# Kernel tuning notes

Measured on AMD Instinct MI355X. Metric: run time of the kernel, lower is better.

## Reference

```python
import jax, jax.numpy as jnp
import numpy as np

V, D, H, NQ = 32000, 768, 12, 768
B, S = 2, 1024
HD = D // H

def conv1d(x, w, b, pad):
    # x [B,C,L], w [O,I,K]
    y = jax.lax.conv_general_dilated(x, w, (1,), [(pad, pad)], dimension_numbers=('NCH', 'OIH', 'NCH'))
    return y + b[None, :, None]

def maxpool3(x):
    return jax.lax.reduce_window(x, -jnp.inf, jax.lax.max, (1, 1, 3), (1, 1, 1), [(0, 0), (0, 0), (1, 1)])

def ln(x, g, b):
    m = jnp.mean(x, -1, keepdims=True)
    v = jnp.mean((x - m) ** 2, -1, keepdims=True)
    return (x - m) * jax.lax.rsqrt(v + 1e-5) * g + b

def setup_inputs():
    key = jax.random.key(0)
    ks = iter(jax.random.split(key, 64))
    def w(shape, s=0.02):
        return jax.random.normal(next(ks), shape, jnp.float32) * s
    inp = {}
    inp['x'] = jax.random.randint(next(ks), (B, S), 0, V)
    inp['attention_mask'] = jax.random.randint(next(ks), (B, S), 0, 2, dtype=jnp.int32)
    inp['adj_matrix'] = jax.random.uniform(next(ks), (B, S, S), jnp.float32) * (1.0 / S)
    inp['emb'] = w((V, D))
    inp['inc1_w'] = w((64, D, 1)); inp['inc1_b'] = jnp.zeros((64,))
    inp['inc3a_w'] = w((96, D, 1)); inp['inc3a_b'] = jnp.zeros((96,))
    inp['inc3b_w'] = w((128, 96, 3)); inp['inc3b_b'] = jnp.zeros((128,))
    inp['inc5a_w'] = w((16, D, 1)); inp['inc5a_b'] = jnp.zeros((16,))
    inp['inc5b_w'] = w((32, 16, 5)); inp['inc5b_b'] = jnp.zeros((32,))
    inp['incp_w'] = w((32, D, 1)); inp['incp_b'] = jnp.zeros((32,))
    inp['q_rot'] = jax.random.normal(next(ks), (2, NQ, 3), jnp.float32)
    inp['q_ent'] = jax.random.normal(next(ks), (2, NQ - 1), jnp.float32)
    inp['gnn_w1'] = w((D, D // 2)); inp['gnn_b1'] = jnp.zeros((D // 2,))
    inp['gnn_w2'] = w((D // 2, D)); inp['gnn_b2'] = jnp.zeros((D,))
    inp['wq'] = w((D, D)); inp['bq'] = jnp.zeros((D,))
    inp['wk'] = w((D, D)); inp['bk'] = jnp.zeros((D,))
    inp['wv'] = w((D, D)); inp['bv'] = jnp.zeros((D,))
    inp['wo'] = w((D, D)); inp['bo'] = jnp.zeros((D,))
    inp['ff_w1'] = w((D, 4 * D)); inp['ff_b1'] = jnp.zeros((4 * D,))
    inp['ff_w2'] = w((4 * D, D)); inp['ff_b2'] = jnp.zeros((D,))
    inp['ln1_g'] = jnp.ones((D,)); inp['ln1_b'] = jnp.zeros((D,))
    inp['ln2_g'] = jnp.ones((D,)); inp['ln2_b'] = jnp.zeros((D,))
    inp['out_w'] = w((D, V)); inp['out_b'] = jnp.zeros((V,))
    inp['task_w'] = w((D, 3)); inp['task_b'] = jnp.zeros((3,))
    return inp

def reference(x, attention_mask, adj_matrix, emb, inc1_w, inc1_b, inc3a_w, inc3a_b, inc3b_w, inc3b_b, inc5a_w, inc5a_b, inc5b_w, inc5b_b, incp_w, incp_b, q_rot, q_ent, gnn_w1, gnn_b1, gnn_w2, gnn_b2, wq, bq, wk, bk, wv, bv, wo, bo, ff_w1, ff_b1, ff_w2, ff_b2, ln1_g, ln1_b, ln2_g, ln2_b, out_w, out_b, task_w, task_b):
    h = emb[x]                      # [B,S,D]
    hc = h.transpose(0, 2, 1)       # [B,D,S]
    b1 = conv1d(hc, inc1_w, inc1_b, 0)
    b3 = conv1d(conv1d(hc, inc3a_w, inc3a_b, 0), inc3b_w, inc3b_b, 1)
    b5 = conv1d(conv1d(hc, inc5a_w, inc5a_b, 0), inc5b_w, inc5b_b, 2)
    bp = conv1d(maxpool3(hc), incp_w, incp_b, 0)
    h = jnp.concatenate([b1, b3, b5, bp], axis=1).transpose(0, 2, 1)  # [B,S,256]
    # quantum layer: pad 256 -> NQ
    h = jnp.pad(h, ((0, 0), (0, 0), (0, NQ - h.shape[-1])))
    for layer in range(2):
        h = jnp.sin(h[..., None] + q_rot[layer]).sum(-1)          # [B,S,NQ]
        hs = jnp.roll(h, 1, axis=-1)
        h = h[..., :-1] * jnp.sin(q_ent[layer]) + hs[..., :-1] * jnp.cos(q_ent[layer])
        h = jnp.pad(h, ((0, 0), (0, 0), (0, 1)))
    # GNN
    g = jax.nn.relu(jnp.matmul(adj_matrix, h) @ gnn_w1 + gnn_b1)
    h = jnp.matmul(adj_matrix, g) @ gnn_w2 + gnn_b2
    # attention (faithful to original mask-bug: masks where transformed mask == 0)
    am = (1.0 - attention_mask.astype(jnp.float32))[:, None, None, :] * -10000.0
    Q = (h @ wq + bq).reshape(B, S, H, HD).transpose(0, 2, 1, 3)
    K = (h @ wk + bk).reshape(B, S, H, HD).transpose(0, 2, 1, 3)
    Vv = (h @ wv + bv).reshape(B, S, H, HD).transpose(0, 2, 1, 3)
    scores = jnp.einsum('bhqd,bhkd->bhqk', Q, K) / jnp.sqrt(jnp.float32(HD))
    scores = jnp.where(am == 0.0, -1e9, scores)
    attn = jax.nn.softmax(scores, axis=-1)
    ctx = jnp.einsum('bhqk,bhkd->bhqd', attn, Vv).transpose(0, 2, 1, 3).reshape(B, S, D)
    h = ln(h + (ctx @ wo + bo), ln1_g, ln1_b)
    ff = jax.nn.relu(h @ ff_w1 + ff_b1) @ ff_w2 + ff_b2
    h = ln(h + ff, ln2_g, ln2_b)
    token_output = h @ out_w + out_b            # [B,S,V]
    task_output = h.mean(axis=1) @ task_w + task_b  # [B,3]
    return token_output, task_output
```

## Files before the change

### kernel.cpp

```cpp
#include <hip/hip_runtime.h>
#include <hip/hip_bf16.h>

#define B_ 2
#define S_ 1024
#define D_ 768
#define H_ 12
#define HD_ 64
#define V_ 32000
#define NQ_ 768
#define NTOK (B_*S_)
#define QKVS 1572864L

typedef __attribute__((ext_vector_type(8))) short short8;
typedef __attribute__((ext_vector_type(4))) short s16x4;
typedef __attribute__((ext_vector_type(4))) float f32x4;
typedef __attribute__((ext_vector_type(4))) int i32x4;

typedef const __attribute__((address_space(1))) void* as1vp;
typedef __attribute__((address_space(3))) void* as3vp;

__device__ __forceinline__ short f2bf(float f) {
    union { float f; unsigned u; } v; v.f = f;
    unsigned r = (v.u + 0x7FFFu + ((v.u >> 16) & 1u)) >> 16;
    return (short)r;
}
__device__ __forceinline__ float b2fs(short s) {
    union { unsigned u; float f; } v; v.u = ((unsigned)(unsigned short)s) << 16;
    return v.f;
}

__global__ void k_embed2(const int* __restrict__ x, const float* __restrict__ emb,
                         short* __restrict__ h0b, short* __restrict__ mpb) {
    int n = blockIdx.x; int s = n & (S_-1);
    int r0 = x[n];
    int rm = (s > 0)      ? x[n-1] : -1;
    int rp = (s < S_-1)   ? x[n+1] : -1;
    for (int d = threadIdx.x; d < D_; d += blockDim.x) {
        float e = emb[(long)r0*D_ + d];
        float m = e;
        if (rm >= 0) m = fmaxf(m, emb[(long)rm*D_ + d]);
        if (rp >= 0) m = fmaxf(m, emb[(long)rp*D_ + d]);
        h0b[(long)n*D_ + d] = f2bf(e);
        mpb[(long)n*D_ + d] = f2bf(m);
    }
}

__global__ __launch_bounds__(256) void k_mix(
    const float* __restrict__ CO, const float* __restrict__ c3w,
    const float* __restrict__ c3b, const float* __restrict__ c5w,
    const float* __restrict__ c5b, const float* __restrict__ q_rot,
    const float* __restrict__ q_ent, float* __restrict__ h1f)
{
    __shared__ float co[5][176];
    __shared__ float ta[NQ_];
    __shared__ float tb[NQ_];
    int n = blockIdx.x; int s = n & (S_-1);
    int t = threadIdx.x;
    for (int idx = t; idx < 5*176; idx += 256) {
        int dr = idx / 176 - 2, c = idx % 176;
        int ss = s + dr;
        co[idx/176][c] = (ss >= 0 && ss < S_) ? CO[(long)(n + dr)*176 + c] : 0.f;
    }
    for (int d = 256 + t; d < NQ_; d += 256) ta[d] = 0.f;
    __syncthreads();
    if (t < 64) {
        ta[t] = co[2][t];
    } else if (t < 192) {
        int o = t - 64;
        float acc = c3b[o];
        #pragma unroll
        for (int k = 0; k < 3; k++)
            for (int i = 0; i < 96; i++)
                acc += co[1+k][64+i] * c3w[(o*96+i)*3 + k];
        ta[t] = acc;
    } else if (t < 224) {
        int o = t - 192;
        float acc = c5b[o];
        #pragma unroll
        for (int k = 0; k < 5; k++)
            for (int i = 0; i < 16; i++)
                acc += co[k][160+i] * c5w[(o*16+i)*5 + k];
        ta[t] = acc;
    } else {
        ta[t] = h1f[(long)n*NQ_ + t];
    }
    __syncthreads();
    #pragma unroll
    for (int layer = 0; layer < 2; layer++) {
        const float* rot = q_rot + (long)layer*NQ_*3;
        const float* ent = q_ent + (long)layer*(NQ_-1);
        for (int q = t; q < NQ_; q += 256) {
            float hv = ta[q];
            tb[q] = __sinf(hv + rot[q*3]) + __sinf(hv + rot[q*3+1]) + __sinf(hv + rot[q*3+2]);
        }
        __syncthreads();
        for (int q = t; q < NQ_; q += 256) {
            float v;
            if (q == NQ_-1) v = 0.f;
            else {
                int qm = (q == 0) ? (NQ_-1) : (q-1);
                v = tb[q]*__sinf(ent[q]) + tb[qm]*__cosf(ent[q]);
            }
            ta[q] = v;
        }
        __syncthreads();
    }
    for (int q = t; q < NQ_; q += 256) h1f[(long)n*NQ_ + q] = ta[q];
}

template<int AMODE, int OMODE, bool RELU, int KSPLIT = 1>
__global__ __launch_bounds__(256) void k_bgemm(
    const short* __restrict__ A, const short* __restrict__ Bm,
    void* __restrict__ Cv, float* __restrict__ C2,
    const float* __restrict__ bias, float scale,
    int N, int K, int lda, int ldb, int ldc,
    long sA, long sB, long sC)
{
    __shared__ short lds[2][8192];
    const int t = threadIdx.x;
    const int lane = t & 63, wave = t >> 6;
    const int wm = wave >> 1, wn = wave & 1;
    const int l15 = lane & 15, l4 = lane >> 4;

    int bx = blockIdx.x, by = blockIdx.y;
    if (KSPLIT == 1 && gridDim.z == 1) {
        int lin = by * gridDim.x + bx;
        int nwg = gridDim.x * gridDim.y;
        int xcd = lin & 7, pos = lin >> 3;
        int q = nwg >> 3, r = nwg & 7;
        int lin2 = (xcd < r ? xcd*(q+1) : r*(q+1) + (xcd-r)*q) + pos;
        bx = lin2 % gridDim.x;
        by = lin2 / gridDim.x;
    }
    const int tile_m = bx * 128, tile_n = by * 128;
    const int kz = (KSPLIT > 1) ? blockIdx.z : 0;
    const int Keff = K / KSPLIT;
    const int kbase = kz * Keff;
    const long aoff = (KSPLIT > 1) ? 0 : (long)blockIdx.z * sA;
    const long boff = (KSPLIT > 1) ? 0 : (long)blockIdx.z * sB;
    const long coff = (KSPLIT > 1) ? 0 : (long)blockIdx.z * sC;

    const int cA0 = t, cA1 = t + 256;
    const int arow0 = tile_m + ((cA0 >> 6) << 4) + (cA0 & 15);
    const int arow1 = tile_m + ((cA1 >> 6) << 4) + (cA1 & 15);
    const int akb0 = ((cA0 >> 4) & 3) * 8;
    const int akb1 = ((cA1 >> 4) & 3) * 8;
    const int bcol0 = tile_n + (((cA0 >> 4) & 7) << 4) + (cA0 & 15);
    const int bcol1 = tile_n + (((cA1 >> 4) & 7) << 4) + (cA1 & 15);
    const int bkb0 = (cA0 >> 7) * 8;
    const int bkb1 = (cA1 >> 7) * 8;
    const short* bp0 = Bm + boff + (long)bcol0*ldb + bkb0 + kbase;
    const short* bp1 = Bm + boff + (long)bcol1*ldb + bkb1 + kbase;
    const short* ap0 = nullptr; const short* ap1 = nullptr;
    long abase0 = 0, abase1 = 0;
    if (AMODE == 0) {
        ap0 = A + aoff + (long)arow0*lda + akb0 + kbase;
        ap1 = A + aoff + (long)arow1*lda + akb1 + kbase;
    } else {
        abase0 = ((long)((arow0 >> 10)*H_) * S_ + (arow0 & (S_-1))) * 64;
        abase1 = ((long)((arow1 >> 10)*H_) * S_ + (arow1 & (S_-1))) * 64;
    }
    const int wb = wave * 1024;

    auto stage = [&](int buf, int k0) {
        char* lb = (char*)&lds[buf][0];
        const short *a0, *a1;
        if (AMODE == 0) { a0 = ap0 + k0; a1 = ap1 + k0; }
        else {
            int ka0 = kbase + k0 + akb0, ka1 = kbase + k0 + akb1;
            a0 = A + abase0 + (long)(ka0 >> 6)*(S_*64) + (ka0 & 63);
            a1 = A + abase1 + (long)(ka1 >> 6)*(S_*64) + (ka1 & 63);
        }
        __builtin_amdgcn_global_load_lds((as1vp)a0,          (as3vp)(lb + wb),          16, 0, 0);
        __builtin_amdgcn_global_load_lds((as1vp)a1,          (as3vp)(lb + 4096 + wb),   16, 0, 0);
        __builtin_amdgcn_global_load_lds((as1vp)(bp0 + k0),  (as3vp)(lb + 8192 + wb),   16, 0, 0);
        __builtin_amdgcn_global_load_lds((as1vp)(bp1 + k0),  (as3vp)(lb + 12288 + wb),  16, 0, 0);
    };

    f32x4 acc[4][4] = {};
    const int nk = Keff >> 5;
    stage(0, 0);
    __syncthreads();
    int cur = 0;
    for (int ks = 0; ks < nk; ks++) {
        if (ks + 1 < nk) stage(cur ^ 1, (ks + 1) << 5);
        short8 af[4], bfv[4];
        const short* lb = &lds[cur][0];
        #pragma unroll
        for (int m = 0; m < 4; m++)
            af[m] = *(const short8*)(lb + (wm*4 + m)*512 + l4*128 + l15*8);
        #pragma unroll
        for (int n = 0; n < 4; n++)
            bfv[n] = *(const short8*)(lb + 4096 + l4*1024 + (wn*4 + n)*128 + l15*8);
        #pragma unroll
        for (int m = 0; m < 4; m++)
            #pragma unroll
            for (int n = 0; n < 4; n++)
                acc[m][n] = __builtin_amdgcn_mfma_f32_16x16x32_bf16(af[m], bfv[n], acc[m][n], 0, 0, 0);
        __syncthreads();
        cur ^= 1;
    }

    #pragma unroll
    for (int m = 0; m < 4; m++) {
        #pragma unroll
        for (int n = 0; n < 4; n++) {
            int col = tile_n + wn*64 + n*16 + l15;
            if (col >= N) continue;
            float bv = (bias && (KSPLIT == 1 || kz == 0)) ? bias[col] : 0.f;
            #pragma unroll
            for (int r = 0; r < 4; r++) {
                int row = tile_m + wm*64 + m*16 + l4*4 + r;
                float v = acc[m][n][r] * scale + bv;
                if (RELU) v = fmaxf(v, 0.f);
                if (OMODE == 0) {
                    if (KSPLIT > 1)
                        atomicAdd(&((float*)Cv)[(long)row*ldc + col], v);
                    else
                        ((float*)Cv)[coff + (long)row*ldc + col] = v;
                } else if (OMODE == 1) {
                    ((short*)Cv)[coff + (long)row*ldc + col] = f2bf(v);
                } else if (OMODE == 2) {
                    C2[coff + (long)row*ldc + col] = v;
                    ((short*)Cv)[coff + (long)row*ldc + col] = f2bf(v);
                } else {
                    int seg = (col >= 1536) ? 2 : ((col >= 768) ? 1 : 0);
                    int c = col - seg*768;
                    int hh = c >> 6, dd = c & 63;
                    int b = row >> 10, s = row & (S_-1);
                    long hidx = (long)(b*H_ + hh);
                    short* base = (short*)Cv;
                    if (seg < 2) base[(long)seg*QKVS + (hidx*S_ + s)*64 + dd] = f2bf(v);
                    else         base[2L*QKVS + (hidx*64 + dd)*S_ + s] = f2bf(v);
                }
            }
        }
    }
}

__global__ __launch_bounds__(512, 1) void k_vgemm(
    const short* __restrict__ A, const short* __restrict__ Bm,
    float* __restrict__ C, const float* __restrict__ bias,
    int N, int K, int lda, int ldb, int ldc)
{
    extern __shared__ short lds[];
    const int t = threadIdx.x;
    const int lane = t & 63, wave = t >> 6;
    const int wm = wave >> 2, wn = wave & 3;
    const int l15 = lane & 15, l4 = lane >> 4;
    int bx = blockIdx.x, by = blockIdx.y;
    {
        int lin = by * gridDim.x + bx;
        int nwg = gridDim.x * gridDim.y;
        int xcd = lin & 7, pos = lin >> 3;
        int q = nwg >> 3, r = nwg & 7;
        int lin2 = (xcd < r ? xcd*(q+1) : r*(q+1) + (xcd-r)*q) + pos;
        bx = lin2 % gridDim.x; by = lin2 / gridDim.x;
    }
    const int tile_m = bx * 256, tile_n = by * 256;

    const int c0 = wave*128 + lane;
    const int c1 = c0 + 64;
    const int ar0 = ((c0 >> 6) << 4) + (c0 & 15), ak0 = ((c0 >> 4) & 3) << 3;
    const int ar1 = ((c1 >> 6) << 4) + (c1 & 15), ak1 = ((c1 >> 4) & 3) << 3;
    const short* pa0 = A + (long)(tile_m + ar0)*lda + ak0;
    const short* pa1 = A + (long)(tile_m + ar1)*lda + ak1;
    const short* pb0 = Bm + (long)(tile_n + ar0)*ldb + ak0;
    const short* pb1 = Bm + (long)(tile_n + ar1)*ldb + ak1;
    char* lb = (char*)lds;
    const int wb0 = wave*2048, wb1 = wave*2048 + 1024;

    auto stage = [&](int reg, int s) {
        int k = s << 5;
        char* ab = lb + reg*32768;
        __builtin_amdgcn_global_load_lds((as1vp)(pa0 + k), (as3vp)(ab + wb0),         16, 0, 0);
        __builtin_amdgcn_global_load_lds((as1vp)(pa1 + k), (as3vp)(ab + wb1),         16, 0, 0);
        __builtin_amdgcn_global_load_lds((as1vp)(pb0 + k), (as3vp)(ab + 16384 + wb0), 16, 0, 0);
        __builtin_amdgcn_global_load_lds((as1vp)(pb1 + k), (as3vp)(ab + 16384 + wb1), 16, 0, 0);
    };

    f32x4 acc[8][4] = {};
    const int nks = K >> 5;
    stage(0, 0); stage(1, 1); stage(2, 2);
    const int ard = ((wm*8) << 10) + (l4 << 8) + l15*16;
    const int brd = 16384 + ((wn*4) << 10) + (l4 << 8) + l15*16;

    int reg = 0;
    for (int s = 0; s < nks; s++) {
        if (s + 3 < nks) {
            int r3 = reg + 3; if (r3 >= 5) r3 -= 5;
            stage(r3, s + 3);
        }
        if (s < nks - 3)       asm volatile("s_waitcnt vmcnt(12)" ::: "memory");
        else if (s == nks - 3) asm volatile("s_waitcnt vmcnt(8)"  ::: "memory");
        else if (s == nks - 2) asm volatile("s_waitcnt vmcnt(4)"  ::: "memory");
        else                   asm volatile("s_waitcnt vmcnt(0)"  ::: "memory");
        __builtin_amdgcn_s_barrier();
        const char* rb = lb + reg*32768;
        short8 a[8], b[4];
        #pragma unroll
        for (int fr = 0; fr < 8; fr++) a[fr] = *(const short8*)(rb + ard + (fr << 10));
        #pragma unroll
        for (int fc = 0; fc < 4; fc++) b[fc] = *(const short8*)(rb + brd + (fc << 10));
        __builtin_amdgcn_s_setprio(1);
        #pragma unroll
        for (int fr = 0; fr < 8; fr++)
            #pragma unroll
            for (int fc = 0; fc < 4; fc++)
                acc[fr][fc] = __builtin_amdgcn_mfma_f32_16x16x32_bf16(a[fr], b[fc], acc[fr][fc], 0, 0, 0);
        __builtin_amdgcn_s_setprio(0);
        if (++reg == 5) reg = 0;
    }

    #pragma unroll
    for (int fr = 0; fr < 8; fr++) {
        #pragma unroll
        for (int fc = 0; fc < 4; fc++) {
            int col = tile_n + wn*64 + fc*16 + l15;
            float bv = bias ? bias[col] : 0.f;
            #pragma unroll
            for (int rr = 0; rr < 4; rr++) {
                int row = tile_m + wm*128 + fr*16 + l4*4 + rr;
                C[(long)row*ldc + col] = acc[fr][fc][rr] + bv;
            }
        }
    }
}

__global__ __launch_bounds__(256) void k_fattn(
    const short* __restrict__ Q, const short* __restrict__ K,
    const short* __restrict__ Vt, const int* __restrict__ mask,
    short* __restrict__ ctx)
{
    __shared__ short plds[4096];
    const int t = threadIdx.x;
    const int lane = t & 63, wave = t >> 6;
    const int l15 = lane & 15, l4 = lane >> 4;
    const int qt = blockIdx.x, z = blockIdx.y;
    const int b = z / H_;
    const long zb = (long)z * S_ * 64;

    const int q = qt*64 + wave*16 + l15;
    short8 aq0 = *(const short8*)(Q + zb + (long)q*64 + l4*8);
    short8 aq1 = *(const short8*)(Q + zb + (long)q*64 + l4*8 + 32);

    float m[4] = {-1e30f, -1e30f, -1e30f, -1e30f};
    float l[4] = {0.f, 0.f, 0.f, 0.f};
    f32x4 O[4] = {};
    short* pw = plds + wave*1024;

    for (int kt = 0; kt < 16; kt++) {
        const int kvb = kt*64;
        f32x4 s[4] = {};
        #pragma unroll
        for (int ct = 0; ct < 4; ct++) {
            const short* kp = K + zb + (long)(kvb + ct*16 + l15)*64 + l4*8;
            short8 b0 = *(const short8*)(kp);
            short8 b1 = *(const short8*)(kp + 32);
            s[ct] = __builtin_amdgcn_mfma_f32_16x16x32_bf16(aq0, b0, s[ct], 0, 0, 0);
            s[ct] = __builtin_amdgcn_mfma_f32_16x16x32_bf16(aq1, b1, s[ct], 0, 0, 0);
        }
        float p[4][4];
        float rmax[4] = {-1e30f, -1e30f, -1e30f, -1e30f};
        #pragma unroll
        for (int ct = 0; ct < 4; ct++) {
            int mv = mask[b*S_ + kvb + ct*16 + l15];
            #pragma unroll
            for (int r = 0; r < 4; r++) {
                float v = (mv == 1) ? -1e9f : s[ct][r]*0.125f;
                p[ct][r] = v;
                rmax[r] = fmaxf(rmax[r], v);
            }
        }
        #pragma unroll
        for (int r = 0; r < 4; r++) {
            float v = rmax[r];
            v = fmaxf(v, __shfl_xor(v, 1));
            v = fmaxf(v, __shfl_xor(v, 2));
            v = fmaxf(v, __shfl_xor(v, 4));
            v = fmaxf(v, __shfl_xor(v, 8));
            float mn = fmaxf(m[r], v);
            float corr = __expf(m[r] - mn);
            float srow = 0.f;
            #pragma unroll
            for (int ct = 0; ct < 4; ct++) {
                float e = __expf(p[ct][r] - mn);
                p[ct][r] = e;
                srow += e;
            }
            srow += __shfl_xor(srow, 1);
            srow += __shfl_xor(srow, 2);
            srow += __shfl_xor(srow, 4);
            srow += __shfl_xor(srow, 8);
            l[r] = l[r]*corr + srow;
            m[r] = mn;
            #pragma unroll
            for (int c2 = 0; c2 < 4; c2++) O[c2][r] *= corr;
        }
        #pragma unroll
        for (int ct = 0; ct < 4; ct++)
            #pragma unroll
            for (int r = 0; r < 4; r++)
                pw[(l4*4 + r)*64 + ct*16 + l15] = f2bf(p[ct][r]);
        asm volatile("s_waitcnt lgkmcnt(0)" ::: "memory");
        __builtin_amdgcn_sched_barrier(0);
        short8 pa0 = *(const short8*)(pw + l15*64 + l4*8);
        short8 pa1 = *(const short8*)(pw + l15*64 + l4*8 + 32);
        #pragma unroll
        for (int c2 = 0; c2 < 4; c2++) {
            const short* vp = Vt + zb + (long)(c2*16 + l15)*S_ + kvb + l4*8;
            short8 v0 = *(const short8*)(vp);
            short8 v1 = *(const short8*)(vp + 32);
            O[c2] = __builtin_amdgcn_mfma_f32_16x16x32_bf16(pa0, v0, O[c2], 0, 0, 0);
            O[c2] = __builtin_amdgcn_mfma_f32_16x16x32_bf16(pa1, v1, O[c2], 0, 0, 0);
        }
    }
    #pragma unroll
    for (int r = 0; r < 4; r++) {
        float inv = 1.f / l[r];
        int qo = qt*64 + wave*16 + l4*4 + r;
        #pragma unroll
        for (int c2 = 0; c2 < 4; c2++)
            ctx[zb + (long)qo*64 + c2*16 + l15] = f2bf(O[c2][r] * inv);
    }
}

struct WPArgs {
    const float *ow, *wq, *wk, *wv, *wo, *g1, *g2, *f1, *f2, *adj;
    const float *w1, *w3, *w5, *wp, *b1, *b3, *b5, *bq, *bk, *bv;
    short *owt, *wqkvt, *gw1t, *gw2t, *fw1t, *fw2t, *adjb, *wincat, *wincp;
    float *binc, *bqkv;
};
__global__ __launch_bounds__(256) void k_wprep(WPArgs a) {
    __shared__ float tile[32][33];
    int blk = blockIdx.x, t = threadIdx.x;
    const float* src; short* dst;
    int R, C, bx, by;
    if (blk < 24000)      { src = a.ow; dst = a.owt; R = 768; C = 32000; bx = blk % 1000; by = blk / 1000; }
    else if (blk < 26304) { int r = blk - 24000; int z = r / 576; r %= 576;
        src = (z == 0) ? a.wq : (z == 1) ? a.wk : (z == 2) ? a.wv : a.wo;
        dst = a.wqkvt + (long)z*589824; R = 768; C = 768; bx = r % 24; by = r / 24; }
    else if (blk < 26592) { int r = blk - 26304; src = a.g1; dst = a.gw1t; R = 768; C = 384;  bx = r % 12; by = r / 12; }
    else if (blk < 26880) { int r = blk - 26592; src = a.g2; dst = a.gw2t; R = 384; C = 768;  bx = r % 24; by = r / 24; }
    else if (blk < 29184) { int r = blk - 26880; src = a.f1; dst = a.fw1t; R = 768; C = 3072; bx = r % 96; by = r / 96; }
    else if (blk < 31488) { int r = blk - 29184; src = a.f2; dst = a.fw2t; R = 3072; C = 768; bx = r % 24; by = r / 24; }
    else if (blk < 33536) {
        long i = ((long)(blk - 31488)*256 + t)*4;
        f32x4 v = *(const f32x4*)(a.adj + i);
        a.adjb[i+0] = f2bf(v.x); a.adjb[i+1] = f2bf(v.y);
        a.adjb[i+2] = f2bf(v.z); a.adjb[i+3] = f2bf(v.w);
        return;
    } else {
        int r = blk - 33536;
        const float* s2; short* d2; long base;
        if (r < 48)       { s2 = a.w1; d2 = a.wincat;          base = (long)r*1024; }
        else if (r < 120) { s2 = a.w3; d2 = a.wincat + 49152;  base = (long)(r-48)*1024; }
        else if (r < 132) { s2 = a.w5; d2 = a.wincat + 122880; base = (long)(r-120)*1024; }
        else if (r < 156) { s2 = a.wp; d2 = a.wincp;           base = (long)(r-132)*1024; }
        else {
            if (t < 176) a.binc[t] = (t < 64) ? a.b1[t] : (t < 160 ? a.b3[t-64] : a.b5[t-160]);
            for (int i = t; i < 2304; i += 256)
                a.bqkv[i] = (i < 768) ? a.bq[i] : (i < 1536 ? a.bk[i-768] : a.bv[i-1536]);
            return;
        }
        long i = base + (long)t*4;
        f32x4 v = *(const f32x4*)(s2 + i);
        d2[i+0] = f2bf(v.x); d2[i+1] = f2bf(v.y); d2[i+2] = f2bf(v.z); d2[i+3] = f2bf(v.w);
        return;
    }
    int bc = bx*32, br = by*32;
    int tx = t & 31, ty = t >> 5;
    #pragma unroll
    for (int i = 0; i < 32; i += 8)
        tile[ty + i][tx] = src[(long)(br + ty + i)*C + bc + tx];
    __syncthreads();
    #pragma unroll
    for (int i = 0; i < 32; i += 8)
        dst[(long)(bc + ty + i)*R + br + tx] = f2bf(tile[tx][ty + i]);
}

template<bool RELU>
__global__ void k_t2b(const float* __restrict__ in, short* __restrict__ out,
                      int R, int C, long sIn, long sOut) {
    __shared__ float tile[32][33];
    int bc = blockIdx.x * 32, br = blockIdx.y * 32;
    const float* ip = in + (long)blockIdx.z * sIn;
    short* op = out + (long)blockIdx.z * sOut;
    int tx = threadIdx.x & 31, ty = threadIdx.x >> 5;
    #pragma unroll
    for (int i = 0; i < 32; i += 8)
        tile[ty + i][tx] = ip[(long)(br + ty + i)*C + bc + tx];
    __syncthreads();
    #pragma unroll
    for (int i = 0; i < 32; i += 8) {
        float v = tile[tx][ty + i];
        if (RELU) v = fmaxf(v, 0.f);
        op[(long)(bc + ty + i)*R + br + tx] = f2bf(v);
    }
}

__global__ void k_addln(const float* __restrict__ a, const float* __restrict__ bvec,
                        const float* __restrict__ g, const float* __restrict__ be,
                        float* __restrict__ outf, short* __restrict__ outb) {
    __shared__ float row[D_];
    __shared__ float red[256];
    int n = blockIdx.x, t = threadIdx.x;
    float lsum = 0.f;
    for (int d = t; d < D_; d += 256) {
        float v = a[(long)n*D_ + d] + bvec[(long)n*D_ + d];
        row[d] = v; lsum += v;
    }
    red[t] = lsum; __syncthreads();
    for (int off = 128; off > 0; off >>= 1) {
        if (t < off) red[t] += red[t+off];
        __syncthreads();
    }
    float mean = red[0] / D_; __syncthreads();
    float lvar = 0.f;
    for (int d = t; d < D_; d += 256) { float v = row[d]-mean; lvar += v*v; }
    red[t] = lvar; __syncthreads();
    for (int off = 128; off > 0; off >>= 1) {
        if (t < off) red[t] += red[t+off];
        __syncthreads();
    }
    float rstd = rsqrtf(red[0]/D_ + 1e-5f);
    for (int d = t; d < D_; d += 256) {
        float v = (row[d]-mean)*rstd*g[d] + be[d];
        if (outf) outf[(long)n*D_ + d] = v;
        outb[(long)n*D_ + d] = f2bf(v);
    }
}

__global__ __launch_bounds__(256) void k_pool(const short* __restrict__ h,
                                              float* __restrict__ pooled) {
    int blk = blockIdx.x;
    int b = blk >> 4, ch = blk & 15;
    int t = threadIdx.x;
    float s0 = 0.f, s1 = 0.f, s2 = 0.f;
    for (int ss = ch*64; ss < ch*64 + 64; ss++) {
        const short* row = h + (long)(b*S_ + ss)*D_;
        s0 += b2fs(row[t]);
        s1 += b2fs(row[t + 256]);
        s2 += b2fs(row[t + 512]);
    }
    atomicAdd(&pooled[b*D_ + t],       s0 * (1.f/S_));
    atomicAdd(&pooled[b*D_ + t + 256], s1 * (1.f/S_));
    atomicAdd(&pooled[b*D_ + t + 512], s2 * (1.f/S_));
}

__global__ __launch_bounds__(256) void k_task(const float* __restrict__ pooled,
                                              const float* __restrict__ tw,
                                              const float* __restrict__ tb,
                                              float* __restrict__ out) {
    __shared__ float red[256][3];
    int b = blockIdx.x, t = threadIdx.x;
    float a0 = 0.f, a1 = 0.f, a2 = 0.f;
    for (int d = t; d < D_; d += 256) {
        float p = pooled[b*D_ + d];
        a0 += p*tw[d*3+0]; a1 += p*tw[d*3+1]; a2 += p*tw[d*3+2];
    }
    red[t][0] = a0; red[t][1] = a1; red[t][2] = a2;
    __syncthreads();
    for (int off = 128; off > 0; off >>= 1) {
        if (t < off) {
            red[t][0] += red[t+off][0];
            red[t][1] += red[t+off][1];
            red[t][2] += red[t+off][2];
        }
        __syncthreads();
    }
    if (t < 3) out[(long)NTOK*V_ + b*3 + t] = red[0][t] + tb[t];
}

extern "C" void kernel_launch(void* const* d_in, const int* in_sizes, int n_in,
                              void* d_out, int out_size, void* d_ws, size_t ws_size,
                              hipStream_t stream) {
    const int*   x      = (const int*)d_in[0];
    const int*   amask  = (const int*)d_in[1];
    const float* adj    = (const float*)d_in[2];
    const float* emb    = (const float*)d_in[3];
    const float* inc1_w = (const float*)d_in[4];  const float* inc1_b = (const float*)d_in[5];
    const float* inc3a_w= (const float*)d_in[6];  const float* inc3a_b= (const float*)d_in[7];
    const float* inc3b_w= (const float*)d_in[8];  const float* inc3b_b= (const float*)d_in[9];
    const float* inc5a_w= (const float*)d_in[10]; const float* inc5a_b= (const float*)d_in[11];
    const float* inc5b_w= (const float*)d_in[12]; const float* inc5b_b= (const float*)d_in[13];
    const float* incp_w = (const float*)d_in[14]; const float* incp_b = (const float*)d_in[15];
    const float* q_rot  = (const float*)d_in[16]; const float* q_ent  = (const float*)d_in[17];
    const float* gnn_w1 = (const float*)d_in[18]; const float* gnn_b1 = (const float*)d_in[19];
    const float* gnn_w2 = (const float*)d_in[20]; const float* gnn_b2 = (const float*)d_in[21];
    const float* wq = (const float*)d_in[22]; const float* bq = (const float*)d_in[23];
    const float* wk = (const float*)d_in[24]; const float* bk = (const float*)d_in[25];
    const float* wv = (const float*)d_in[26]; const float* bv = (const float*)d_in[27];
    const float* wo = (const float*)d_in[28]; const float* bo = (const float*)d_in[29];
    const float* ff_w1 = (const float*)d_in[30]; const float* ff_b1 = (const float*)d_in[31];
    const float* ff_w2 = (const float*)d_in[32]; const float* ff_b2 = (const float*)d_in[33];
    const float* ln1_g = (const float*)d_in[34]; const float* ln1_b = (const float*)d_in[35];
    const float* ln2_g = (const float*)d_in[36]; const float* ln2_b = (const float*)d_in[37];
    const float* out_w = (const float*)d_in[38]; const float* out_b = (const float*)d_in[39];
    const float* task_w= (const float*)d_in[40]; const float* task_b= (const float*)d_in[41];

    float* F = (float*)d_out;
    short* wqkvt = (short*)(F + 0L);
    short* gw1t  = (short*)(F + 1179648L);
    short* gw2t  = (short*)(F + 1327104L);
    short* fw1t  = (short*)(F + 1474560L);
    short* fw2t  = (short*)(F + 2654208L);
    short* wincat= (short*)(F + 3833856L);
    short* wincp = (short*)(F + 3950592L);
    float* binc  = F + 4012032L;
    float* bqkv  = F + 4012288L;
    short* adjb  = (short*)(F + 4014592L);
    short* h0b   = (short*)(F + 5063168L);
    short* mpb   = (short*)(F + 5849600L);
    float* CO    = F + 6636032L;
    float* h1f   = F + 6996480L;
    short* h1t   = (short*)(F + 8569344L);
    short* t1b   = (short*)(F + 9355776L);
    float* gbf   = F + 10142208L;
    short* gt    = (short*)(F + 10928640L);
    short* t2bv  = (short*)(F + 11321856L);
    float* h2f   = F + 11715072L;
    short* h2b   = (short*)(F + 13287936L);
    short* Qh    = (short*)(F + 14074368L);
    short* Kh    = (short*)(F + 14860800L);
    short* Vt    = (short*)(F + 15647232L);
    short* ctxh  = (short*)(F + 16499200L);
    float* ao    = F + 17285632L;
    float* hlnf  = F + 18858496L;
    short* hlnb  = (short*)(F + 20431360L);
    short* ff1b  = (short*)(F + 21217792L);
    float* ao2   = F + 24363520L;

    char* W = (char*)d_ws;
    short* hfb    = (short*)(W + 0);
    float* pooled = (float*)(W + 3145728);
    short* owt    = (short*)(W + 3151872);

    auto gb = [](int M, int N, int Z) { return dim3((unsigned)(M/128), (unsigned)((N+127)/128), (unsigned)Z); };

    hipFuncSetAttribute((const void*)k_vgemm, hipFuncAttributeMaxDynamicSharedMemorySize, 163840);

    hipMemsetAsync(gbf, 0, (size_t)NTOK*384*4, stream);
    hipMemsetAsync(ao,  0, (size_t)NTOK*D_*4, stream);
    hipMemsetAsync(ao2, 0, (size_t)NTOK*D_*4, stream);
    hipMemsetAsync(CO,  0, (size_t)NTOK*176*4, stream);
    hipMemsetAsync(h1f, 0, (size_t)NTOK*NQ_*4, stream);
    hipMemsetAsync(pooled, 0, (size_t)B_*D_*4, stream);

    {
        WPArgs wa;
        wa.ow = out_w; wa.wq = wq; wa.wk = wk; wa.wv = wv; wa.wo = wo;
        wa.g1 = gnn_w1; wa.g2 = gnn_w2; wa.f1 = ff_w1; wa.f2 = ff_w2; wa.adj = adj;
        wa.w1 = inc1_w; wa.w3 = inc3a_w; wa.w5 = inc5a_w; wa.wp = incp_w;
        wa.b1 = inc1_b; wa.b3 = inc3a_b; wa.b5 = inc5a_b;
        wa.bq = bq; wa.bk = bk; wa.bv = bv;
        wa.owt = owt; wa.wqkvt = wqkvt; wa.gw1t = gw1t; wa.gw2t = gw2t;
        wa.fw1t = fw1t; wa.fw2t = fw2t; wa.adjb = adjb;
        wa.wincat = wincat; wa.wincp = wincp; wa.binc = binc; wa.bqkv = bqkv;
        k_wprep<<<dim3(33693), 256, 0, stream>>>(wa);
    }

    k_embed2<<<dim3(NTOK), dim3(256), 0, stream>>>(x, emb, h0b, mpb);

    k_bgemm<0,0,false,4><<<gb(NTOK, 176, 4), 256, 0, stream>>>(
        h0b, wincat, CO, nullptr, binc, 1.f, 176, D_, D_, D_, 176, 0, 0, 0);
    k_bgemm<0,0,false,8><<<gb(NTOK, 32, 8), 256, 0, stream>>>(
        mpb, wincp, h1f + 224, nullptr, incp_b, 1.f, 32, D_, D_, D_, NQ_, 0, 0, 0);

    k_mix<<<dim3(NTOK), dim3(256), 0, stream>>>(
        CO, inc3b_w, inc3b_b, inc5b_w, inc5b_b, q_rot, q_ent, h1f);

    k_t2b<false><<<dim3(24,32,2), 256, 0, stream>>>(h1f, h1t, S_, NQ_, (long)S_*NQ_, (long)S_*NQ_);
    k_bgemm<0,1,false><<<gb(S_, NQ_, B_), 256, 0, stream>>>(
        adjb, h1t, t1b, nullptr, nullptr, 1.f, NQ_, S_, S_, S_, NQ_,
        (long)S_*S_, (long)NQ_*S_, (long)S_*NQ_);
    k_bgemm<0,0,false,4><<<gb(NTOK, 384, 4), 256, 0, stream>>>(
        t1b, gw1t, gbf, nullptr, gnn_b1, 1.f, 384, D_, D_, D_, 384, 0, 0, 0);
    k_t2b<true><<<dim3(12,32,2), 256, 0, stream>>>(gbf, gt, S_, 384, (long)S_*384, (long)S_*384);
    k_bgemm<0,1,false><<<gb(S_, 384, B_), 256, 0, stream>>>(
        adjb, gt, t2bv, nullptr, nullptr, 1.f, 384, S_, S_, S_, 384,
        (long)S_*S_, (long)384*S_, (long)S_*384);
    k_bgemm<0,2,false><<<gb(NTOK, D_, 1), 256, 0, stream>>>(
        t2bv, gw2t, h2b, h2f, gnn_b2, 1.f, D_, 384, 384, 384, D_, 0, 0, 0);

    k_bgemm<0,5,false><<<gb(NTOK, 3*D_, 1), 256, 0, stream>>>(
        h2b, wqkvt, Qh, nullptr, bqkv, 1.f, 3*D_, D_, D_, D_, 0, 0, 0, 0);
    k_fattn<<<dim3(S_/64, B_*H_), 256, 0, stream>>>(Qh, Kh, Vt, amask, ctxh);
    k_bgemm<1,0,false,2><<<gb(NTOK, D_, 2), 256, 0, stream>>>(
        ctxh, wqkvt + 3L*589824, ao, nullptr, bo, 1.f, D_, D_, D_, D_, D_, 0, 0, 0);
    k_addln<<<dim3(NTOK), dim3(256), 0, stream>>>(h2f, ao, ln1_g, ln1_b, hlnf, hlnb);

    k_bgemm<0,1,true><<<gb(NTOK, 4*D_, 1), 256, 0, stream>>>(
        hlnb, fw1t, ff1b, nullptr, ff_b1, 1.f, 4*D_, D_, D_, D_, 4*D_, 0, 0, 0);
    k_bgemm<0,0,false,4><<<gb(NTOK, D_, 4), 256, 0, stream>>>(
        ff1b, fw2t, ao2, nullptr, ff_b2, 1.f, D_, 4*D_, 4*D_, 4*D_, D_, 0, 0, 0);
    k_addln<<<dim3(NTOK), dim3(256), 0, stream>>>(hlnf, ao2, ln2_g, ln2_b, nullptr, hfb);

    k_pool<<<dim3(B_*16), dim3(256), 0, stream>>>(hfb, pooled);
    k_vgemm<<<dim3(NTOK/256, V_/256, 1), dim3(512), 163840, stream>>>(
        hfb, owt, (float*)d_out, out_b, V_, D_, D_, D_, V_);
    k_task<<<dim3(B_), dim3(256), 0, stream>>>(pooled, task_w, task_b, (float*)d_out);
}
```

Before: 640.2 us.

## Restructure vocab GEMM pipeline to double-buffered 64-wide K phases

Replaces the five-slot, three-deep staged pipeline (32-wide K steps with fine-grained vmcnt waits) in the output-vocabulary GEMM with a two-buffer scheme. Each buffer holds a 64-wide K chunk, and each phase does one full wait and barrier, then runs two MFMA sub-steps. This halves the barrier count per K and cuts dynamic LDS from 160KB to 128KB. The trade is a shallower prefetch: each phase now waits for all outstanding loads (vmcnt 0), so memory latency may be less hidden.

New measurement: 650.1 us. No clear change (+1.6%).

```diff
diff --git a/kernel.cpp b/kernel.cpp
--- a/kernel.cpp
+++ b/kernel.cpp
@@ -270,46 +270,47 @@
     char* lb = (char*)lds;
     const int wb0 = wave*2048, wb1 = wave*2048 + 1024;
 
-    auto stage = [&](int reg, int s) {
-        int k = s << 5;
-        char* ab = lb + reg*32768;
-        __builtin_amdgcn_global_load_lds((as1vp)(pa0 + k), (as3vp)(ab + wb0),         16, 0, 0);
-        __builtin_amdgcn_global_load_lds((as1vp)(pa1 + k), (as3vp)(ab + wb1),         16, 0, 0);
-        __builtin_amdgcn_global_load_lds((as1vp)(pb0 + k), (as3vp)(ab + 16384 + wb0), 16, 0, 0);
-        __builtin_amdgcn_global_load_lds((as1vp)(pb1 + k), (as3vp)(ab + 16384 + wb1), 16, 0, 0);
+    auto stage = [&](int reg, int p) {
+        int k = p << 6;
+        char* ab = lb + reg*65536;
+        __builtin_amdgcn_global_load_lds((as1vp)(pa0 + k),      (as3vp)(ab + wb0),          16, 0, 0);
+        __builtin_amdgcn_global_load_lds((as1vp)(pa1 + k),      (as3vp)(ab + wb1),          16, 0, 0);
+        __builtin_amdgcn_global_load_lds((as1vp)(pa0 + k + 32), (as3vp)(ab + 16384 + wb0),  16, 0, 0);
+        __builtin_amdgcn_global_load_lds((as1vp)(pa1 + k + 32), (as3vp)(ab + 16384 + wb1),  16, 0, 0);
+        __builtin_amdgcn_global_load_lds((as1vp)(pb0 + k),      (as3vp)(ab + 32768 + wb0),  16, 0, 0);
+        __builtin_amdgcn_global_load_lds((as1vp)(pb1 + k),      (as3vp)(ab + 32768 + wb1),  16, 0, 0);
+        __builtin_amdgcn_global_load_lds((as1vp)(pb0 + k + 32), (as3vp)(ab + 49152 + wb0),  16, 0, 0);
+        __builtin_amdgcn_global_load_lds((as1vp)(pb1 + k + 32), (as3vp)(ab + 49152 + wb1),  16, 0, 0);
     };
 
     f32x4 acc[8][4] = {};
-    const int nks = K >> 5;
-    stage(0, 0); stage(1, 1); stage(2, 2);
+    const int nph = K >> 6;
+    stage(0, 0);
     const int ard = ((wm*8) << 10) + (l4 << 8) + l15*16;
-    const int brd = 16384 + ((wn*4) << 10) + (l4 << 8) + l15*16;
-
-    int reg = 0;
-    for (int s = 0; s < nks; s++) {
-        if (s + 3 < nks) {
-            int r3 = reg + 3; if (r3 >= 5) r3 -= 5;
-            stage(r3, s + 3);
-        }
-        if (s < nks - 3)       asm volatile("s_waitcnt vmcnt(12)" ::: "memory");
-        else if (s == nks - 3) asm volatile("s_waitcnt vmcnt(8)"  ::: "memory");
-        else if (s == nks - 2) asm volatile("s_waitcnt vmcnt(4)"  ::: "memory");
-        else                   asm volatile("s_waitcnt vmcnt(0)"  ::: "memory");
+    const int brd = 32768 + ((wn*4) << 10) + (l4 << 8) + l15*16;
+
+    for (int p = 0; p < nph; p++) {
+        asm volatile("s_waitcnt vmcnt(0)" ::: "memory");
         __builtin_amdgcn_s_barrier();
-        const char* rb = lb + reg*32768;
-        short8 a[8], b[4];
-        #pragma unroll
-        for (int fr = 0; fr < 8; fr++) a[fr] = *(const short8*)(rb + ard + (fr << 10));
-        #pragma unroll
-        for (int fc = 0; fc < 4; fc++) b[fc] = *(const short8*)(rb + brd + (fc << 10));
-        __builtin_amdgcn_s_setprio(1);
-        #pragma unroll
-        for (int fr = 0; fr < 8; fr++)
+        if (p + 1 < nph) stage((p + 1) & 1, p + 1);
+        const char* rb = lb + (p & 1)*65536;
+        #pragma unroll
+        for (int h = 0; h < 2; h++) {
+            short8 a[8], b[4];
+            #pragma unroll
+            for (int fr = 0; fr < 8; fr++)
+                a[fr] = *(const short8*)(rb + h*16384 + ard + (fr << 10));
             #pragma unroll
             for (int fc = 0; fc < 4; fc++)
-                acc[fr][fc] = __builtin_amdgcn_mfma_f32_16x16x32_bf16(a[fr], b[fc], acc[fr][fc], 0, 0, 0);
-        __builtin_amdgcn_s_setprio(0);
-        if (++reg == 5) reg = 0;
+                b[fc] = *(const short8*)(rb + h*16384 + brd + (fc << 10));
+            __builtin_amdgcn_s_setprio(1);
+            #pragma unroll
+            for (int fr = 0; fr < 8; fr++)
+                #pragma unroll
+                for (int fc = 0; fc < 4; fc++)
+                    acc[fr][fc] = __builtin_amdgcn_mfma_f32_16x16x32_bf16(a[fr], b[fc], acc[fr][fc], 0, 0, 0);
+            __builtin_amdgcn_s_setprio(0);
+        }
     }
 
     #pragma unroll
@@ -638,7 +639,7 @@
 
     auto gb = [](int M, int N, int Z) { return dim3((unsigned)(M/128), (unsigned)((N+127)/128), (unsigned)Z); };
 
-    hipFuncSetAttribute((const void*)k_vgemm, hipFuncAttributeMaxDynamicSharedMemorySize, 163840);
+    hipFuncSetAttribute((const void*)k_vgemm, hipFuncAttributeMaxDynamicSharedMemorySize, 131072);
 
     hipMemsetAsync(gbf, 0, (size_t)NTOK*384*4, stream);
     hipMemsetAsync(ao,  0, (size_t)NTOK*D_*4, stream);
@@ -697,7 +698,7 @@
     k_addln<<<dim3(NTOK), dim3(256), 0, stream>>>(hlnf, ao2, ln2_g, ln2_b, nullptr, hfb);
 
     k_pool<<<dim3(B_*16), dim3(256), 0, stream>>>(hfb, pooled);
-    k_vgemm<<<dim3(NTOK/256, V_/256, 1), dim3(512), 163840, stream>>>(
+    k_vgemm<<<dim3(NTOK/256, V_/256, 1), dim3(512), 131072, stream>>>(
         hfb, owt, (float*)d_out, out_b, V_, D_, D_, D_, V_);
     k_task<<<dim3(B_), dim3(256), 0, stream>>>(pooled, task_w, task_b, (float*)d_out);
 }
```
